# Kernel tuning notes

Hardware: AMD Instinct MI355X
Metric: run time of the kernel (lower is better)

The kernel has to match this reference:

```python
import jax, jax.numpy as jnp
import numpy as np

B_, C_, H_, W_ = 32, 1, 512, 512
SMOOTH = 1.0


def _neighbors(im):
    # im: (N, H, W) bool. Returns the 8 neighbors P2..P9 (Zhang-Suen ordering:
    # N, NE, E, SE, S, SW, W, NW), zero-padded at the border.
    p = jnp.pad(im, ((0, 0), (1, 1), (1, 1)))
    P2 = p[:, :-2, 1:-1]
    P3 = p[:, :-2, 2:]
    P4 = p[:, 1:-1, 2:]
    P5 = p[:, 2:, 2:]
    P6 = p[:, 2:, 1:-1]
    P7 = p[:, 2:, :-2]
    P8 = p[:, 1:-1, :-2]
    P9 = p[:, :-2, :-2]
    return P2, P3, P4, P5, P6, P7, P8, P9


def _subiter(im, first: bool):
    P2, P3, P4, P5, P6, P7, P8, P9 = _neighbors(im)
    nb = [P2, P3, P4, P5, P6, P7, P8, P9]
    Bcnt = sum(n.astype(jnp.int32) for n in nb)          # number of set neighbors
    seq = nb + [P2]
    A = sum(((~seq[i]) & seq[i + 1]).astype(jnp.int32) for i in range(8))  # 0->1 transitions
    if first:
        cond = (~(P2 & P4 & P6)) & (~(P4 & P6 & P8))
    else:
        cond = (~(P2 & P4 & P8)) & (~(P2 & P6 & P8))
    remove = im & (Bcnt >= 2) & (Bcnt <= 6) & (A == 1) & cond
    return im & (~remove)


def _skeletonize(im):
    # Zhang-Suen thinning (the 2D algorithm skimage.morphology.skeletonize uses),
    # iterated to convergence. im: (N, H, W) bool.
    def body(state):
        cur, _ = state
        nxt = _subiter(_subiter(cur, True), False)
        return nxt, jnp.any(nxt != cur)

    def cond_fn(state):
        return state[1]

    out, _ = jax.lax.while_loop(cond_fn, body, (im, jnp.array(True)))
    return out


def _dilate_cross(im):
    # skimage.morphology.dilation with default cross-shaped (connectivity-1) footprint.
    p = jnp.pad(im, ((0, 0), (1, 1), (1, 1)))
    return im | p[:, :-2, 1:-1] | p[:, 2:, 1:-1] | p[:, 1:-1, :-2] | p[:, 1:-1, 2:]


def _skeleton_tube(y):
    # y: (B, C, H, W) int. Returns float skeleton (dilated twice) same shape.
    Bn, C, H, W = y.shape
    mask = y.reshape(Bn * C, H, W) > 0
    skel = _skeletonize(mask)
    skel = _dilate_cross(_dilate_cross(skel))
    return skel.reshape(Bn, C, H, W).astype(jnp.float32)


def setup_inputs() -> dict:
    key = jax.random.key(0)
    k1, k2 = jax.random.split(key)
    x = jax.random.uniform(k1, (B_, C_, H_, W_), dtype=jnp.float32)  # probabilities (apply_nonlin=None)
    y = jax.random.randint(k2, (B_, C_, H_, W_), 0, 2, dtype=jnp.int32)  # binary GT mask
    return {"x": x, "y": y}


def reference(x, y):
    y_skel = _skeleton_tube(y)                     # (B, C, H, W) float, constant wrt x
    axes = (2, 3)
    intersection = (x * y_skel).sum(axis=axes)     # (B, C)
    gt_sum = y_skel.sum(axis=axes)                 # (B, C)
    recall = (intersection + SMOOTH) / (gt_sum + SMOOTH)
    return -recall.mean()
```

## Files before the change

### kernel.cpp

```cpp
#include <hip/hip_runtime.h>
#include <stdint.h>

typedef unsigned long long u64;
typedef unsigned int u32;

#define BATCH 32
#define H 512
#define W 512
#define WPR 8
#define WORDS_IMG (H * WPR)
#define NPIX (H * W)

#define NSTRIP 8
#define OWN 64
#define NBLK (BATCH * NSTRIP)

#define HALO1 32
#define RL1 128
#define PAIRS1 16
#define THR1 512

#define WP 9
#define ERL 68

__global__ __launch_bounds__(256) void pack_kernel(const int* __restrict__ y,
                                                   u64* __restrict__ words,
                                                   int* __restrict__ flags,
                                                   int* __restrict__ counter) {
    if (blockIdx.x == 0 && threadIdx.x == 0) { flags[0] = 0; counter[0] = 0; }
    int gtid = blockIdx.x * blockDim.x + threadIdx.x;
    int lane = gtid & 63;
    int wave = gtid >> 6;
    const int* yb = y + (size_t)wave * 16 * 64;
    u64* wb = words + (size_t)wave * 16;
    int v[16];
    #pragma unroll
    for (int i = 0; i < 16; ++i) v[i] = yb[i * 64 + lane];
    #pragma unroll
    for (int i = 0; i < 16; ++i) {
        u64 m = __ballot(v[i] != 0);
        if (lane == 0) wb[i] = m;
    }
}

__device__ __forceinline__ void fulladd(u64 a, u64 b, u64 c, u64& s, u64& cy) {
    u64 t = a ^ b;
    s = t ^ c;
    cy = (a & b) | (t & c);
}

template<bool FIRST, int RLp>
__device__ __forceinline__ u64 subiter2(const u64* __restrict__ src,
                                        u64* __restrict__ dst,
                                        int rg, int wc) {
    const int r = 2 * rg;
    u64 C[4], L[4], R[4];
    #pragma unroll
    for (int i = 0; i < 4; ++i) {
        int rr = r - 1 + i;
        bool v = (rr >= 0) && (rr < RLp);
        const u64* row = src + rr * WP;
        C[i] = v ? row[wc] : 0ull;
        L[i] = (v && wc > 0) ? row[wc - 1] : 0ull;
        R[i] = (v && wc < 7) ? row[wc + 1] : 0ull;
    }
    u64 Wst[4], Est[4];
    #pragma unroll
    for (int i = 0; i < 4; ++i) {
        Wst[i] = (C[i] << 1) | (L[i] >> 63);
        Est[i] = (C[i] >> 1) | (R[i] << 63);
    }
    u64 diff = 0;
    #pragma unroll
    for (int k = 0; k < 2; ++k) {
        u64 P2 = C[k],     P9 = Wst[k],     P3 = Est[k];
        u64 cC = C[k + 1], P8 = Wst[k + 1], P4 = Est[k + 1];
        u64 P6 = C[k + 2], P7 = Wst[k + 2], P5 = Est[k + 2];

        u64 s1, c1, s2, c2, s3, c3, ts, tc, us, uc;
        fulladd(P2, P3, P4, s1, c1);
        fulladd(P5, P6, P7, s2, c2);
        s3 = P8 ^ P9; c3 = P8 & P9;
        fulladd(s1, s2, s3, ts, tc);
        fulladd(c1, c2, c3, us, uc);
        u64 vs = us ^ tc, vc = us & tc;
        u64 w4 = uc ^ vc, w8 = uc & vc;
        u64 condB = (vs | w4 | w8) & ~(w8 | (w4 & vs & ts));

        u64 seen, multi, t;
        t = ~P2 & P3; seen = t;  multi = 0;
        t = ~P3 & P4; multi |= seen & t; seen |= t;
        t = ~P4 & P5; multi |= seen & t; seen |= t;
        t = ~P5 & P6; multi |= seen & t; seen |= t;
        t = ~P6 & P7; multi |= seen & t; seen |= t;
        t = ~P7 & P8; multi |= seen & t; seen |= t;
        t = ~P8 & P9; multi |= seen & t; seen |= t;
        t = ~P9 & P2; multi |= seen & t; seen |= t;
        u64 ex1 = seen & ~multi;

        u64 cond = FIRST ? (~(P2 & P4 & P6) & ~(P4 & P6 & P8))
                         : (~(P2 & P4 & P8) & ~(P2 & P6 & P8));

        u64 rem = cC & condB & ex1 & cond;
        u64 nw = cC & ~rem;
        dst[(r + k) * WP + wc] = nw;
        diff |= nw ^ cC;
    }
    return diff;
}

__global__ __launch_bounds__(THR1)
void strip16(const u64* __restrict__ gsrc, u64* __restrict__ gdst,
             int* __restrict__ flags) {
    __shared__ u64 A[RL1 * WP];
    __shared__ u64 Bf[RL1 * WP];
    __shared__ int s_any[2];

    const int tid = threadIdx.x;
    const int blk = blockIdx.x;
    const int b = blk >> 3;
    const int s = blk & 7;
    const int row0 = s * OWN;
    const int lane = tid & 63;
    const u64* src = gsrc + (size_t)b * WORDS_IMG;
    u64* dst = gdst + (size_t)b * WORDS_IMG;

    #pragma unroll
    for (int i = 0; i < 2; ++i) {
        int t = tid + i * THR1;
        int lrow = t >> 3, c = t & 7;
        int grow = row0 - HALO1 + lrow;
        u64 v = 0;
        if (grow >= 0 && grow < H) v = src[grow * WPR + c];
        A[lrow * WP + c] = v;
    }
    if (tid < 2) s_any[tid] = 0;
    __syncthreads();

    const int rg = tid >> 3;
    const int wc = tid & 7;
    u64 lastown = 0;
    for (int pr = 0; pr < PAIRS1; ++pr) {
        const int lo = 2 * pr + 1;
        const int hi = 126 - 2 * pr;
        const bool active = (2 * rg + 1 >= lo) && (2 * rg <= hi);
        u64 d1 = 0, d2 = 0;
        if (active) d1 = subiter2<true, RL1>(A, Bf, rg, wc);
        __syncthreads();
        if (active) d2 = subiter2<false, RL1>(Bf, A, rg, wc);
        u64 d = d1 | d2;
        lastown = (rg >= 16 && rg < 48) ? d : 0;
        int p = pr & 1;
        u64 bal = __ballot(d != 0);
        if (lane == 0 && bal) atomicOr(&s_any[p], 1);
        __syncthreads();
        int any = s_any[p];
        if (tid == 0) s_any[p ^ 1] = 0;
        if (!any) break;
    }

    if (rg >= 16 && rg < 48) {
        int r = 2 * rg;
        dst[(row0 + r - HALO1) * WPR + wc]     = A[r * WP + wc];
        dst[(row0 + r - HALO1 + 1) * WPR + wc] = A[(r + 1) * WP + wc];
    }
    u64 bal = __ballot(lastown != 0);
    if (lane == 0 && bal) atomicOr(&flags[0], 1);
}

template<bool FIRST>
__device__ __forceinline__ void compute_sub_full(const u64* img, int wc, int r0,
                                                 u64 nw[8], u64& diff) {
    u64 C[10], L[10], R[10];
    #pragma unroll
    for (int i = 0; i < 10; ++i) {
        int rr = r0 - 1 + i;
        bool valid = (rr >= 0) && (rr < H);
        C[i] = valid ? img[rr * WPR + wc] : 0ull;
        L[i] = (valid && wc > 0) ? img[rr * WPR + wc - 1] : 0ull;
        R[i] = (valid && wc < WPR - 1) ? img[rr * WPR + wc + 1] : 0ull;
    }
    #pragma unroll
    for (int k = 0; k < 8; ++k) {
        u64 P2 = C[k];
        u64 P9 = (C[k]   << 1) | (L[k]   >> 63);
        u64 P3 = (C[k]   >> 1) | (R[k]   << 63);
        u64 cC = C[k+1];
        u64 P8 = (C[k+1] << 1) | (L[k+1] >> 63);
        u64 P4 = (C[k+1] >> 1) | (R[k+1] << 63);
        u64 P6 = C[k+2];
        u64 P7 = (C[k+2] << 1) | (L[k+2] >> 63);
        u64 P5 = (C[k+2] >> 1) | (R[k+2] << 63);

        u64 s1, c1, s2, c2, s3, c3, ts, tc, us, uc;
        fulladd(P2, P3, P4, s1, c1);
        fulladd(P5, P6, P7, s2, c2);
        s3 = P8 ^ P9; c3 = P8 & P9;
        fulladd(s1, s2, s3, ts, tc);
        fulladd(c1, c2, c3, us, uc);
        u64 vs = us ^ tc, vc = us & tc;
        u64 w4 = uc ^ vc, w8 = uc & vc;
        u64 condB = (vs | w4 | w8) & ~(w8 | (w4 & vs & ts));

        u64 seen, multi, t;
        t = ~P2 & P3; seen = t;  multi = 0;
        t = ~P3 & P4; multi |= seen & t; seen |= t;
        t = ~P4 & P5; multi |= seen & t; seen |= t;
        t = ~P5 & P6; multi |= seen & t; seen |= t;
        t = ~P6 & P7; multi |= seen & t; seen |= t;
        t = ~P7 & P8; multi |= seen & t; seen |= t;
        t = ~P8 & P9; multi |= seen & t; seen |= t;
        t = ~P9 & P2; multi |= seen & t; seen |= t;
        u64 ex1 = seen & ~multi;

        u64 cond = FIRST ? (~(P2 & P4 & P6) & ~(P4 & P6 & P8))
                         : (~(P2 & P4 & P8) & ~(P2 & P6 & P8));

        u64 rem = cC & condB & ex1 & cond;
        nw[k] = cC & ~rem;
        diff |= nw[k] ^ cC;
    }
}

__global__ __launch_bounds__(512)
void fullfix_kernel(u64* __restrict__ gimg0, const int* __restrict__ flags) {
    if (flags[0] == 0) return;

    __shared__ u64 img[WORDS_IMG];
    __shared__ int s_changed;
    const int b = blockIdx.x;
    const int tid = threadIdx.x;
    const int wc = tid & 7;
    const int r0 = (tid >> 3) * 8;
    u64* gimg = gimg0 + (size_t)b * WORDS_IMG;

    #pragma unroll
    for (int k = 0; k < 8; ++k)
        img[(r0 + k) * WPR + wc] = gimg[(r0 + k) * WPR + wc];
    if (tid == 0) s_changed = 0;
    __syncthreads();

    bool changed = true;
    for (int it = 0; it < 4096 && changed; ++it) {
        u64 diff = 0;
        u64 nw[8];
        compute_sub_full<true>(img, wc, r0, nw, diff);
        __syncthreads();
        #pragma unroll
        for (int k = 0; k < 8; ++k) img[(r0 + k) * WPR + wc] = nw[k];
        __syncthreads();
        compute_sub_full<false>(img, wc, r0, nw, diff);
        __syncthreads();
        #pragma unroll
        for (int k = 0; k < 8; ++k) img[(r0 + k) * WPR + wc] = nw[k];
        if (diff) atomicOr(&s_changed, 1);
        __syncthreads();
        changed = (s_changed != 0);
        __syncthreads();
        if (tid == 0) s_changed = 0;
    }

    #pragma unroll
    for (int k = 0; k < 8; ++k)
        gimg[(r0 + k) * WPR + wc] = img[(r0 + k) * WPR + wc];
}

__global__ __launch_bounds__(512)
void tail_kernel(const u64* __restrict__ gB, const float* __restrict__ x,
                 float* __restrict__ partial, int* __restrict__ partial_gt,
                 int* __restrict__ counter, float* __restrict__ out) {
    __shared__ u64 D[ERL * WP];
    __shared__ u64 E[ERL * WP];
    __shared__ float s_red[8];
    __shared__ int s_pc[8];
    __shared__ int s_last;

    const int tid = threadIdx.x;
    const int blk = blockIdx.x;
    const int b = blk >> 3;
    const int s = blk & 7;
    const int row0 = s * OWN;
    const int lane = tid & 63;
    const int wv = tid >> 6;
    const u64* src = gB + (size_t)b * WORDS_IMG;

    const float4* x4 = (const float4*)(x + (size_t)b * NPIX + (size_t)row0 * W);
    const int quad = tid & 127;
    const int rgp  = tid >> 7;
    float4 xv[16];
    #pragma unroll
    for (int i = 0; i < 16; ++i)
        xv[i] = x4[(i * 4 + rgp) * 128 + quad];

    for (int t = tid; t < ERL * 8; t += 512) {
        int lrow = t >> 3, c = t & 7;
        int grow = row0 - 2 + lrow;
        u64 v = 0;
        if (grow >= 0 && grow < H) v = src[grow * WPR + c];
        D[lrow * WP + c] = v;
    }
    __syncthreads();

    for (int t = tid; t < ERL * 8; t += 512) {
        int l = t >> 3, c = t & 7;
        int grow = row0 - 2 + l;
        u64 v = 0;
        if (grow >= 0 && grow < H) {
            u64 cc = D[l * WP + c];
            u64 up = (l > 0)       ? D[(l - 1) * WP + c] : 0ull;
            u64 dn = (l < ERL - 1) ? D[(l + 1) * WP + c] : 0ull;
            u64 lw = (c > 0) ? D[l * WP + c - 1] : 0ull;
            u64 rw = (c < 7) ? D[l * WP + c + 1] : 0ull;
            v = cc | up | dn | ((cc << 1) | (lw >> 63)) | ((cc >> 1) | (rw << 63));
        }
        E[l * WP + c] = v;
    }
    __syncthreads();

    const int l = 2 + (tid >> 3);
    const int c = tid & 7;
    u64 v;
    {
        u64 cc = E[l * WP + c];
        u64 up = E[(l - 1) * WP + c];
        u64 dn = E[(l + 1) * WP + c];
        u64 lw = (c > 0) ? E[l * WP + c - 1] : 0ull;
        u64 rw = (c < 7) ? E[l * WP + c + 1] : 0ull;
        v = cc | up | dn | ((cc << 1) | (lw >> 63)) | ((cc >> 1) | (rw << 63));
    }
    int pc = __popcll(v);
    for (int off = 32; off >= 1; off >>= 1) pc += __shfl_down(pc, off, 64);
    if (lane == 0) s_pc[wv] = pc;
    __syncthreads();
    D[l * WP + c] = v;
    __syncthreads();

    const int wi = quad >> 4;
    const int sh = (quad & 15) * 4;
    float s0 = 0.0f, s1 = 0.0f, s2 = 0.0f, s3 = 0.0f;
    #pragma unroll
    for (int i = 0; i < 16; ++i) {
        int rrow = i * 4 + rgp;
        u64 word = D[(2 + rrow) * WP + wi];
        u32 bits = (u32)(word >> sh) & 0xFu;
        s0 = fmaf((float)(bits & 1u),        xv[i].x, s0);
        s1 = fmaf((float)((bits >> 1) & 1u), xv[i].y, s1);
        s2 = fmaf((float)((bits >> 2) & 1u), xv[i].z, s2);
        s3 = fmaf((float)((bits >> 3) & 1u), xv[i].w, s3);
    }
    float sum = (s0 + s1) + (s2 + s3);
    for (int off = 32; off >= 1; off >>= 1) sum += __shfl_down(sum, off, 64);
    if (lane == 0) s_red[wv] = sum;
    __syncthreads();

    if (tid == 0) {
        float fs = 0.0f;
        int is = 0;
        #pragma unroll
        for (int k = 0; k < 8; ++k) { fs += s_red[k]; is += s_pc[k]; }
        __hip_atomic_store(&partial[blk], fs, __ATOMIC_RELAXED,
                           __HIP_MEMORY_SCOPE_AGENT);
        __hip_atomic_store(&partial_gt[blk], is, __ATOMIC_RELAXED,
                           __HIP_MEMORY_SCOPE_AGENT);
        int prev = __hip_atomic_fetch_add(counter, 1, __ATOMIC_ACQ_REL,
                                          __HIP_MEMORY_SCOPE_AGENT);
        s_last = (prev == NBLK - 1);
    }
    __syncthreads();

    if (s_last && tid < 32) {
        float inter = 0.0f;
        int g = 0;
        #pragma unroll
        for (int j = 0; j < 8; ++j) {
            inter += __hip_atomic_load(&partial[tid * 8 + j], __ATOMIC_RELAXED,
                                       __HIP_MEMORY_SCOPE_AGENT);
            g += __hip_atomic_load(&partial_gt[tid * 8 + j], __ATOMIC_RELAXED,
                                   __HIP_MEMORY_SCOPE_AGENT);
        }
        float rec = (inter + 1.0f) / ((float)g + 1.0f);
        #pragma unroll
        for (int off = 16; off >= 1; off >>= 1)
            rec += __shfl_down(rec, off, 32);
        if (tid == 0) out[0] = -(rec / 32.0f);
    }
}

extern "C" void kernel_launch(void* const* d_in, const int* in_sizes, int n_in,
                              void* d_out, int out_size, void* d_ws, size_t ws_size,
                              hipStream_t stream) {
    const float* x = (const float*)d_in[0];
    const int*   y = (const int*)d_in[1];
    float* out = (float*)d_out;

    char* ws = (char*)d_ws;
    u64* gA = (u64*)ws;
    u64* gB = (u64*)(ws + (size_t)BATCH * WORDS_IMG * 8);
    int* flags = (int*)(ws + 2 * (size_t)BATCH * WORDS_IMG * 8);
    int* counter = flags + 4;
    float* partial = (float*)(counter + 4);
    int* partial_gt = (int*)(partial + NBLK);

    pack_kernel<<<2048, 256, 0, stream>>>(y, gA, flags, counter);
    strip16<<<NBLK, THR1, 0, stream>>>(gA, gB, flags);
    fullfix_kernel<<<BATCH, 512, 0, stream>>>(gB, flags);
    tail_kernel<<<NBLK, 512, 0, stream>>>(gB, x, partial, partial_gt,
                                          counter, out);
}
```

Baseline: 44.25 us.

## Fold fallback full-image thinning into tail kernel and vectorize mask packing

Removes the separate fullfix kernel launch. Each tail block now redundantly runs the full-image thinning fallback in shared memory when the flag is set, and otherwise reads the strip result directly. The pack kernel switches to int4 loads with ballots and a bit-spread interleave to build the 64-bit words. This saves one launch and its global round trip, at the cost of 8x redundant fallback work per image and much larger shared memory use in the tail kernel, which may reduce occupancy.

```diff
diff --git a/kernel.cpp b/kernel.cpp
--- a/kernel.cpp
+++ b/kernel.cpp
@@ -22,6 +22,14 @@
 
 #define WP 9
 #define ERL 68
+
+__device__ __forceinline__ u64 spread4(u64 x) {
+    x = (x | (x << 24)) & 0x000000FF000000FFull;
+    x = (x | (x << 12)) & 0x000F000F000F000Full;
+    x = (x | (x << 6))  & 0x0303030303030303ull;
+    x = (x | (x << 3))  & 0x1111111111111111ull;
+    return x;
+}
 
 __global__ __launch_bounds__(256) void pack_kernel(const int* __restrict__ y,
                                                    u64* __restrict__ words,
@@ -31,16 +39,36 @@
     int gtid = blockIdx.x * blockDim.x + threadIdx.x;
     int lane = gtid & 63;
     int wave = gtid >> 6;
-    const int* yb = y + (size_t)wave * 16 * 64;
+    const int4* y4 = (const int4*)y;
     u64* wb = words + (size_t)wave * 16;
-    int v[16];
-    #pragma unroll
-    for (int i = 0; i < 16; ++i) v[i] = yb[i * 64 + lane];
-    #pragma unroll
-    for (int i = 0; i < 16; ++i) {
-        u64 m = __ballot(v[i] != 0);
-        if (lane == 0) wb[i] = m;
-    }
+
+    int4 v[4];
+    #pragma unroll
+    for (int i = 0; i < 4; ++i)
+        v[i] = y4[(size_t)wave * 256 + i * 64 + lane];
+
+    u64 b[4][4];
+    #pragma unroll
+    for (int i = 0; i < 4; ++i) {
+        u32 n = (v[i].x != 0 ? 1u : 0u) | (v[i].y != 0 ? 2u : 0u)
+              | (v[i].z != 0 ? 4u : 0u) | (v[i].w != 0 ? 8u : 0u);
+        b[i][0] = __ballot((n & 1u) != 0);
+        b[i][1] = __ballot((n & 2u) != 0);
+        b[i][2] = __ballot((n & 4u) != 0);
+        b[i][3] = __ballot((n & 8u) != 0);
+    }
+
+    const int j = lane & 3;
+    u64 Wrd = 0;
+    #pragma unroll
+    for (int c = 0; c < 4; ++c) {
+        u64 s0 = (lane & 4) ? b[1][c] : b[0][c];
+        u64 s1 = (lane & 4) ? b[3][c] : b[2][c];
+        u64 bs = (lane & 8) ? s1 : s0;
+        u64 u = (bs >> (j << 4)) & 0xFFFFull;
+        Wrd |= spread4(u) << c;
+    }
+    if (lane < 16) wb[lane] = Wrd;
 }
 
 __device__ __forceinline__ void fulladd(u64 a, u64 b, u64 c, u64& s, u64& cy) {
@@ -223,57 +251,17 @@
 }
 
 __global__ __launch_bounds__(512)
-void fullfix_kernel(u64* __restrict__ gimg0, const int* __restrict__ flags) {
-    if (flags[0] == 0) return;
-
-    __shared__ u64 img[WORDS_IMG];
-    __shared__ int s_changed;
-    const int b = blockIdx.x;
-    const int tid = threadIdx.x;
-    const int wc = tid & 7;
-    const int r0 = (tid >> 3) * 8;
-    u64* gimg = gimg0 + (size_t)b * WORDS_IMG;
-
-    #pragma unroll
-    for (int k = 0; k < 8; ++k)
-        img[(r0 + k) * WPR + wc] = gimg[(r0 + k) * WPR + wc];
-    if (tid == 0) s_changed = 0;
-    __syncthreads();
-
-    bool changed = true;
-    for (int it = 0; it < 4096 && changed; ++it) {
-        u64 diff = 0;
-        u64 nw[8];
-        compute_sub_full<true>(img, wc, r0, nw, diff);
-        __syncthreads();
-        #pragma unroll
-        for (int k = 0; k < 8; ++k) img[(r0 + k) * WPR + wc] = nw[k];
-        __syncthreads();
-        compute_sub_full<false>(img, wc, r0, nw, diff);
-        __syncthreads();
-        #pragma unroll
-        for (int k = 0; k < 8; ++k) img[(r0 + k) * WPR + wc] = nw[k];
-        if (diff) atomicOr(&s_changed, 1);
-        __syncthreads();
-        changed = (s_changed != 0);
-        __syncthreads();
-        if (tid == 0) s_changed = 0;
-    }
-
-    #pragma unroll
-    for (int k = 0; k < 8; ++k)
-        gimg[(r0 + k) * WPR + wc] = img[(r0 + k) * WPR + wc];
-}
-
-__global__ __launch_bounds__(512)
-void tail_kernel(const u64* __restrict__ gB, const float* __restrict__ x,
+void tail_kernel(const u64* __restrict__ gB, const int* __restrict__ flags,
+                 const float* __restrict__ x,
                  float* __restrict__ partial, int* __restrict__ partial_gt,
                  int* __restrict__ counter, float* __restrict__ out) {
+    __shared__ u64 img[WORDS_IMG];
     __shared__ u64 D[ERL * WP];
     __shared__ u64 E[ERL * WP];
     __shared__ float s_red[8];
     __shared__ int s_pc[8];
     __shared__ int s_last;
+    __shared__ int s_changed;
 
     const int tid = threadIdx.x;
     const int blk = blockIdx.x;
@@ -292,11 +280,40 @@
     for (int i = 0; i < 16; ++i)
         xv[i] = x4[(i * 4 + rgp) * 128 + quad];
 
+    const int ff = flags[0];
+    if (ff) {
+        const int wc2 = tid & 7;
+        const int r02 = (tid >> 3) * 8;
+        for (int t = tid; t < WORDS_IMG; t += 512) img[t] = src[t];
+        if (tid == 0) s_changed = 0;
+        __syncthreads();
+        bool changed = true;
+        for (int it = 0; it < 4096 && changed; ++it) {
+            u64 diff = 0;
+            u64 nw[8];
+            compute_sub_full<true>(img, wc2, r02, nw, diff);
+            __syncthreads();
+            #pragma unroll
+            for (int k = 0; k < 8; ++k) img[(r02 + k) * WPR + wc2] = nw[k];
+            __syncthreads();
+            compute_sub_full<false>(img, wc2, r02, nw, diff);
+            __syncthreads();
+            #pragma unroll
+            for (int k = 0; k < 8; ++k) img[(r02 + k) * WPR + wc2] = nw[k];
+            if (diff) atomicOr(&s_changed, 1);
+            __syncthreads();
+            changed = (s_changed != 0);
+            __syncthreads();
+            if (tid == 0) s_changed = 0;
+        }
+    }
+
     for (int t = tid; t < ERL * 8; t += 512) {
         int lrow = t >> 3, c = t & 7;
         int grow = row0 - 2 + lrow;
         u64 v = 0;
-        if (grow >= 0 && grow < H) v = src[grow * WPR + c];
+        if (grow >= 0 && grow < H)
+            v = ff ? img[grow * WPR + c] : src[grow * WPR + c];
         D[lrow * WP + c] = v;
     }
     __syncthreads();
@@ -403,7 +420,6 @@
 
     pack_kernel<<<2048, 256, 0, stream>>>(y, gA, flags, counter);
     strip16<<<NBLK, THR1, 0, stream>>>(gA, gB, flags);
-    fullfix_kernel<<<BATCH, 512, 0, stream>>>(gB, flags);
-    tail_kernel<<<NBLK, 512, 0, stream>>>(gB, x, partial, partial_gt,
+    tail_kernel<<<NBLK, 512, 0, stream>>>(gB, flags, x, partial, partial_gt,
                                           counter, out);
 }
```

After: 53.59 us. +21.1%, slower.
